# Optimization experiments

Measured on AMD Instinct MI355X. Metric: run time of the kernel, lower is better.

## Reference

```python
import jax, jax.numpy as jnp
import numpy as np

B, S, D = 4, 2048, 768
H = 12
HD = D // H  # 64


def setup_inputs() -> dict:
    key = jax.random.key(0)
    ks = jax.random.split(key, 7)
    scale = 1.0 / np.sqrt(D)
    return {
        "hidden_states": jax.random.normal(ks[0], (B, S, D), dtype=jnp.float32),
        "Wq": jax.random.normal(ks[1], (D, D), dtype=jnp.float32) * scale,
        "bq": jnp.zeros((D,), dtype=jnp.float32),
        "Wk": jax.random.normal(ks[2], (D, D), dtype=jnp.float32) * scale,
        "bk": jnp.zeros((D,), dtype=jnp.float32),
        "Wv": jax.random.normal(ks[3], (D, D), dtype=jnp.float32) * scale,
        "bv": jnp.zeros((D,), dtype=jnp.float32),
    }


def _split_heads(x):
    # [B, S, D] -> [B, H, S, HD]
    b, s, _ = x.shape
    return x.reshape(b, s, H, HD).transpose(0, 2, 1, 3)


def reference(hidden_states, Wq, bq, Wk, bk, Wv, bv):
    q = _split_heads(hidden_states @ Wq + bq)
    k = _split_heads(hidden_states @ Wk + bk)
    v = _split_heads(hidden_states @ Wv + bv)
    # [B, H, S, S] attention scores (naive full materialization, as in source)
    scores = jnp.einsum("bhqd,bhkd->bhqk", q, k) / jnp.sqrt(jnp.float32(HD))
    attn = jax.nn.softmax(scores, axis=-1)  # dropout = identity (eval)
    ctx = jnp.einsum("bhqk,bhkd->bhqd", attn, v)
    # [B, H, S, HD] -> [B, S, D]
    return ctx.transpose(0, 2, 1, 3).reshape(hidden_states.shape[0], -1, H * HD)
```

## Files before the change

### kernel.cpp

```cpp
#include <hip/hip_runtime.h>
#include <cmath>

#define B_  4
#define S_  2048
#define D_  768
#define H_  12
#define HD_ 64
#define BH_ 48
#define N3_ 2304
#define M_  8192

typedef _Float16 half8  __attribute__((ext_vector_type(8)));
typedef _Float16 half4v __attribute__((ext_vector_type(4)));
typedef __fp16   fp16x2 __attribute__((ext_vector_type(2)));
typedef __fp16   fp16x4 __attribute__((ext_vector_type(4)));
typedef float    floatx4 __attribute__((ext_vector_type(4)));

typedef const unsigned int __attribute__((address_space(1)))* gas_u32;
typedef unsigned int __attribute__((address_space(3)))* las_u32;

#define LOG2E 1.4426950408889634f
#define NEG_C (-5.0f * 1.4426950408889634f)

__global__ void cvt_f32_f16(const float* __restrict__ src,
                            _Float16* __restrict__ dst, int n) {
  int i = (blockIdx.x * blockDim.x + threadIdx.x) * 4;
  if (i < n) {
    float4 v = *(const float4*)(src + i);
    half4v h = {(_Float16)v.x, (_Float16)v.y, (_Float16)v.z, (_Float16)v.w};
    *(half4v*)(dst + i) = h;
  }
}

__global__ __launch_bounds__(256) void transpose_cvt_w(
    const float* __restrict__ W, _Float16* __restrict__ Wt) {
  __shared__ float tile[32][33];
  const int k0 = blockIdx.x * 32, n0 = blockIdx.y * 32;
  const int r = threadIdx.x >> 3, c4 = (threadIdx.x & 7) * 4;
  float4 v = *(const float4*)(W + (size_t)(k0 + r) * D_ + n0 + c4);
  tile[r][c4 + 0] = v.x; tile[r][c4 + 1] = v.y;
  tile[r][c4 + 2] = v.z; tile[r][c4 + 3] = v.w;
  __syncthreads();
  half4v h = {(_Float16)tile[c4 + 0][r], (_Float16)tile[c4 + 1][r],
              (_Float16)tile[c4 + 2][r], (_Float16)tile[c4 + 3][r]};
  *(half4v*)(Wt + (size_t)(n0 + r) * D_ + k0 + c4) = h;
}

__global__ __launch_bounds__(256, 3) void gemm_qkv(
    const _Float16* __restrict__ Xh, const _Float16* __restrict__ Wt3,
    const float* __restrict__ bq, const float* __restrict__ bk,
    const float* __restrict__ bv,
    _Float16* __restrict__ qo, _Float16* __restrict__ ko,
    _Float16* __restrict__ vto) {
  __shared__ __align__(16) char gsm[36864];
  _Float16* As = (_Float16*)gsm;
  _Float16* Bs = (_Float16*)(gsm + 16384);
  const int tid = threadIdx.x;
  const int w = tid >> 6, lane = tid & 63;
  const int tx = lane & 15, quad = lane >> 4;
  const int nBase = blockIdx.x * 128;
  const int mBase = blockIdx.y * 128;
  const int wm = (w & 1) * 64, wn = (w >> 1) * 64;

  floatx4 acc[4][4];
  #pragma unroll
  for (int i = 0; i < 4; ++i)
    #pragma unroll
    for (int j = 0; j < 4; ++j) acc[i][j] = (floatx4){0.f, 0.f, 0.f, 0.f};

  const int ldRow = lane >> 3;
  const int ldCol = (lane & 7) * 8;

  for (int k0 = 0; k0 < D_; k0 += 64) {
    __syncthreads();
    #pragma unroll
    for (int io = 0; io < 4; ++io) {
      int row = w * 32 + io * 8;
      const _Float16* ga =
          Xh + (size_t)(mBase + row + ldRow) * D_ + k0 + ldCol;
      __builtin_amdgcn_global_load_lds((gas_u32)(const void*)ga,
                                       (las_u32)(void*)&As[row * 64], 16, 0, 0);
      const _Float16* gb =
          Wt3 + (size_t)(nBase + row + ldRow) * D_ + k0 + ldCol;
      __builtin_amdgcn_global_load_lds((gas_u32)(const void*)gb,
                                       (las_u32)(void*)&Bs[row * 64], 16, 0, 0);
    }
    __syncthreads();

    half8 af0[4], af1[4], bf0[4], bf1[4];
    #pragma unroll
    for (int i = 0; i < 4; ++i) {
      af0[i] = *(const half8*)&As[(wm + 16 * i + tx) * 64 + quad * 8];
      af1[i] = *(const half8*)&As[(wm + 16 * i + tx) * 64 + quad * 8 + 32];
    }
    #pragma unroll
    for (int j = 0; j < 4; ++j) {
      bf0[j] = *(const half8*)&Bs[(wn + 16 * j + tx) * 64 + quad * 8];
      bf1[j] = *(const half8*)&Bs[(wn + 16 * j + tx) * 64 + quad * 8 + 32];
    }
    #pragma unroll
    for (int i = 0; i < 4; ++i)
      #pragma unroll
      for (int j = 0; j < 4; ++j) {
        acc[i][j] = __builtin_amdgcn_mfma_f32_16x16x32_f16(af0[i], bf0[j], acc[i][j], 0, 0, 0);
        acc[i][j] = __builtin_amdgcn_mfma_f32_16x16x32_f16(af1[i], bf1[j], acc[i][j], 0, 0, 0);
      }
  }

  const int region = nBase / 768;
  const int b = mBase >> 11;
  const int sBase = mBase & (S_ - 1);

  if (region < 2) {
    const float scale = (region == 0) ? 0.125f * LOG2E : 1.0f;
    const float* bias = (region == 0) ? bq : bk;
    _Float16* dst = (region == 0) ? qo : ko;
    const int nLoc768 = nBase % 768;
    __syncthreads();
    _Float16 (*Ct)[136] = (_Float16(*)[136])gsm;
    #pragma unroll
    for (int j = 0; j < 4; ++j) {
      int nl = wn + 16 * j + tx;
      float bb = bias[nLoc768 + nl];
      #pragma unroll
      for (int i = 0; i < 4; ++i)
        #pragma unroll
        for (int r = 0; r < 4; ++r)
          Ct[wm + 16 * i + quad * 4 + r][nl] = (_Float16)((acc[i][j][r] + bb) * scale);
    }
    __syncthreads();
    #pragma unroll
    for (int io = 0; io < 8; ++io) {
      int idx = io * 256 + tid;
      int ml = idx >> 4;
      int nc = (idx & 15) * 8;
      int n = nLoc768 + nc, h = n >> 6, d = n & 63;
      half8 hv = *(const half8*)&Ct[ml][nc];
      *(half8*)(dst + ((size_t)(b * H_ + h) * S_ + sBase + ml) * HD_ + d) = hv;
    }
  } else {
    __syncthreads();
    _Float16 (*Ct)[144] = (_Float16(*)[144])gsm;
    const int nV = nBase - 1536;
    #pragma unroll
    for (int j = 0; j < 4; ++j) {
      int nl = wn + 16 * j + tx;
      float bb = bv[nV + nl];
      #pragma unroll
      for (int i = 0; i < 4; ++i)
        #pragma unroll
        for (int r = 0; r < 4; ++r)
          Ct[nl][wm + 16 * i + quad * 4 + r] = (_Float16)(acc[i][j][r] + bb);
    }
    __syncthreads();
    #pragma unroll
    for (int io = 0; io < 8; ++io) {
      int idx = io * 256 + tid;
      int nl = idx >> 4;
      int sc = (idx & 15) * 8;
      int n = nV + nl, h = n >> 6, d = n & 63;
      half8 hv = *(const half8*)&Ct[nl][sc];
      *(half8*)(vto + (((size_t)(b * H_ + h) * HD_) + d) * S_ + sBase + sc) = hv;
    }
  }
}

__global__ __launch_bounds__(512, 4) void attn_mfma(
    const _Float16* __restrict__ qh, const _Float16* __restrict__ kh,
    const _Float16* __restrict__ vth, float* __restrict__ out) {
  __shared__ __align__(16) char smem[36864];
  _Float16 (*Ks2)[64][72]  = (_Float16(*)[64][72])smem;
  _Float16 (*Vts2)[64][72] = (_Float16(*)[64][72])(smem + 18432);
  float (*Of)[68] = (float(*)[68])smem;
  float* lbuf = (float*)(smem + 34816);

  const int tid = threadIdx.x;
  const int bh = blockIdx.y;
  const int qBase = blockIdx.x * 128;
  const int w = tid >> 6, lane = tid & 63;
  const int half = w >> 2, wq = w & 3;
  const int tx = lane & 15, quad = lane >> 4;

  const _Float16* kp = kh + (size_t)bh * S_ * HD_;
  const _Float16* vtp = vth + (size_t)bh * HD_ * S_;

  half8 bq[2][2];
  #pragma unroll
  for (int g = 0; g < 2; ++g) {
    const _Float16* qp =
        qh + ((size_t)bh * S_ + qBase + wq * 32 + g * 16 + tx) * HD_;
    bq[g][0] = *(const half8*)(qp + quad * 8);
    bq[g][1] = *(const half8*)(qp + quad * 8 + 32);
  }

  floatx4 o_acc[2][4];
  #pragma unroll
  for (int g = 0; g < 2; ++g)
    #pragma unroll
    for (int j = 0; j < 4; ++j) o_acc[g][j] = (floatx4){0.f, 0.f, 0.f, 0.f};
  float l_loc[2] = {0.f, 0.f};

  const int th = tid & 255;
  const int kr = th >> 3, kc = (th & 7) * 8;

  for (int it = 0; it < S_ / 128; ++it) {
    const int kt0 = it * 128 + half * 64;
    __syncthreads();
    #pragma unroll
    for (int io = 0; io < 2; ++io) {
      int row = kr + io * 32;
      *(half8*)&Ks2[half][row][kc] =
          *(const half8*)(kp + (size_t)(kt0 + row) * HD_ + kc);
      *(half8*)&Vts2[half][row][kc] =
          *(const half8*)(vtp + (size_t)row * S_ + kt0 + kc);
    }
    __syncthreads();

    #pragma unroll
    for (int t = 0; t < 4; ++t) {
      half8 ka0 = *(const half8*)&Ks2[half][16 * t + tx][quad * 8];
      half8 ka1 = *(const half8*)&Ks2[half][16 * t + tx][quad * 8 + 32];
      fp16x4 pf[2];
      #pragma unroll
      for (int g = 0; g < 2; ++g) {
        __builtin_amdgcn_s_setprio(1);
        floatx4 st = __builtin_amdgcn_mfma_f32_16x16x32_f16(
            ka0, bq[g][0], (floatx4){NEG_C, NEG_C, NEG_C, NEG_C}, 0, 0, 0);
        st = __builtin_amdgcn_mfma_f32_16x16x32_f16(ka1, bq[g][1], st, 0, 0, 0);
        __builtin_amdgcn_s_setprio(0);
        float p0 = __builtin_amdgcn_exp2f(st[0]);
        float p1 = __builtin_amdgcn_exp2f(st[1]);
        float p2 = __builtin_amdgcn_exp2f(st[2]);
        float p3 = __builtin_amdgcn_exp2f(st[3]);
        l_loc[g] += (p0 + p1) + (p2 + p3);
        fp16x2 lo = __builtin_amdgcn_cvt_pkrtz(p0, p1);
        fp16x2 hi = __builtin_amdgcn_cvt_pkrtz(p2, p3);
        pf[g] = (fp16x4){lo.x, lo.y, hi.x, hi.y};
      }
      __builtin_amdgcn_s_setprio(1);
      #pragma unroll
      for (int j = 0; j < 4; ++j) {
        fp16x4 vb = *(const fp16x4*)&Vts2[half][16 * j + tx][16 * t + quad * 4];
        o_acc[0][j] = __builtin_amdgcn_mfma_f32_16x16x16f16(pf[0], vb, o_acc[0][j], 0, 0, 0);
        o_acc[1][j] = __builtin_amdgcn_mfma_f32_16x16x16f16(pf[1], vb, o_acc[1][j], 0, 0, 0);
      }
      __builtin_amdgcn_s_setprio(0);
    }
  }

  float lg[2];
  #pragma unroll
  for (int g = 0; g < 2; ++g) {
    lg[g] = l_loc[g];
    lg[g] += __shfl_xor(lg[g], 16, 64);
    lg[g] += __shfl_xor(lg[g], 32, 64);
  }

  __syncthreads();
  if (half == 1) {
    #pragma unroll
    for (int g = 0; g < 2; ++g) {
      int rowB = wq * 32 + g * 16;
      #pragma unroll
      for (int j = 0; j < 4; ++j)
        #pragma unroll
        for (int r = 0; r < 4; ++r)
          Of[rowB + quad * 4 + r][16 * j + tx] = o_acc[g][j][r];
      if (quad == 0) lbuf[rowB + tx] = lg[g];
    }
  }
  __syncthreads();
  if (half == 0) {
    const int b = bh / H_;
    const int h = bh % H_;
    #pragma unroll
    for (int g = 0; g < 2; ++g) {
      int rowB = wq * 32 + g * 16;
      float ltot = lg[g] + lbuf[rowB + tx];
      #pragma unroll
      for (int r = 0; r < 4; ++r) {
        int m = quad * 4 + r;
        float inv = 1.f / __shfl(ltot, m, 64);
        int s = qBase + rowB + m;
        #pragma unroll
        for (int j = 0; j < 4; ++j) {
          float o = o_acc[g][j][r] + Of[rowB + m][16 * j + tx];
          out[((size_t)b * S_ + s) * D_ + h * HD_ + 16 * j + tx] = o * inv;
        }
      }
    }
  }
}

extern "C" void kernel_launch(void* const* d_in, const int* in_sizes, int n_in,
                              void* d_out, int out_size, void* d_ws, size_t ws_size,
                              hipStream_t stream) {
  const float* X  = (const float*)d_in[0];
  const float* Wq = (const float*)d_in[1];
  const float* bq = (const float*)d_in[2];
  const float* Wk = (const float*)d_in[3];
  const float* bk = (const float*)d_in[4];
  const float* Wv = (const float*)d_in[5];
  const float* bv = (const float*)d_in[6];
  float* out = (float*)d_out;

  const size_t nX = (size_t)M_ * D_;
  const size_t nW = (size_t)D_ * D_;
  const size_t nQ = (size_t)BH_ * S_ * HD_;

  _Float16* Xh  = (_Float16*)d_ws;
  _Float16* Wt3 = Xh + nX;
  _Float16* qhb = Wt3 + 3 * nW;
  _Float16* khb = qhb + nQ;
  _Float16* vtb = khb + nQ;

  cvt_f32_f16<<<(int)(nX / 4 / 256), 256, 0, stream>>>(X, Xh, (int)nX);

  dim3 gridT(D_ / 32, D_ / 32);
  transpose_cvt_w<<<gridT, 256, 0, stream>>>(Wq, Wt3);
  transpose_cvt_w<<<gridT, 256, 0, stream>>>(Wk, Wt3 + nW);
  transpose_cvt_w<<<gridT, 256, 0, stream>>>(Wv, Wt3 + 2 * nW);

  dim3 gridG(N3_ / 128, M_ / 128);
  gemm_qkv<<<gridG, 256, 0, stream>>>(Xh, Wt3, bq, bk, bv, qhb, khb, vtb);

  dim3 gridA(S_ / 128, BH_);
  attn_mfma<<<gridA, 512, 0, stream>>>(qhb, khb, vtb, out);
}
```

Before: 212.7 us.

## Register-prefetch next K/V tile in attention loop and merge weight transposes

The attention kernel now loads the next K and V^T tile from global memory into registers while the current tile is being computed, then writes them to shared memory at the start of the next iteration. This hides global load latency behind the MFMA and softmax work. The three weight transpose-convert launches are merged into a single launch with a z-dimension selecting the matrix, which saves two kernel launches. The cost is extra registers per thread, which could reduce occupancy.

```diff
diff --git a/kernel.cpp b/kernel.cpp
--- a/kernel.cpp
+++ b/kernel.cpp
@@ -32,9 +32,13 @@
   }
 }
 
-__global__ __launch_bounds__(256) void transpose_cvt_w(
-    const float* __restrict__ W, _Float16* __restrict__ Wt) {
+__global__ __launch_bounds__(256) void transpose_cvt_w3(
+    const float* __restrict__ Wq, const float* __restrict__ Wk,
+    const float* __restrict__ Wv, _Float16* __restrict__ Wt3) {
   __shared__ float tile[32][33];
+  const int which = blockIdx.z;
+  const float* W = (which == 0) ? Wq : (which == 1) ? Wk : Wv;
+  _Float16* Wt = Wt3 + (size_t)which * D_ * D_;
   const int k0 = blockIdx.x * 32, n0 = blockIdx.y * 32;
   const int r = threadIdx.x >> 3, c4 = (threadIdx.x & 7) * 4;
   float4 v = *(const float4*)(W + (size_t)(k0 + r) * D_ + n0 + c4);
@@ -203,16 +207,34 @@
   const int th = tid & 255;
   const int kr = th >> 3, kc = (th & 7) * 8;
 
-  for (int it = 0; it < S_ / 128; ++it) {
-    const int kt0 = it * 128 + half * 64;
-    __syncthreads();
+  const int NT = S_ / 128;
+  half8 kst[2], vst[2];
+  {
+    const int kt0 = half * 64;
     #pragma unroll
     for (int io = 0; io < 2; ++io) {
       int row = kr + io * 32;
-      *(half8*)&Ks2[half][row][kc] =
-          *(const half8*)(kp + (size_t)(kt0 + row) * HD_ + kc);
-      *(half8*)&Vts2[half][row][kc] =
-          *(const half8*)(vtp + (size_t)row * S_ + kt0 + kc);
+      kst[io] = *(const half8*)(kp + (size_t)(kt0 + row) * HD_ + kc);
+      vst[io] = *(const half8*)(vtp + (size_t)row * S_ + kt0 + kc);
+    }
+  }
+
+  for (int it = 0; it < NT; ++it) {
+    __syncthreads();
+    #pragma unroll
+    for (int io = 0; io < 2; ++io) {
+      int row = kr + io * 32;
+      *(half8*)&Ks2[half][row][kc] = kst[io];
+      *(half8*)&Vts2[half][row][kc] = vst[io];
+    }
+    if (it + 1 < NT) {
+      const int kt1 = (it + 1) * 128 + half * 64;
+      #pragma unroll
+      for (int io = 0; io < 2; ++io) {
+        int row = kr + io * 32;
+        kst[io] = *(const half8*)(kp + (size_t)(kt1 + row) * HD_ + kc);
+        vst[io] = *(const half8*)(vtp + (size_t)row * S_ + kt1 + kc);
+      }
     }
     __syncthreads();
 
@@ -316,10 +338,8 @@
 
   cvt_f32_f16<<<(int)(nX / 4 / 256), 256, 0, stream>>>(X, Xh, (int)nX);
 
-  dim3 gridT(D_ / 32, D_ / 32);
-  transpose_cvt_w<<<gridT, 256, 0, stream>>>(Wq, Wt3);
-  transpose_cvt_w<<<gridT, 256, 0, stream>>>(Wk, Wt3 + nW);
-  transpose_cvt_w<<<gridT, 256, 0, stream>>>(Wv, Wt3 + 2 * nW);
+  dim3 gridT(D_ / 32, D_ / 32, 3);
+  transpose_cvt_w3<<<gridT, 256, 0, stream>>>(Wq, Wk, Wv, Wt3);
 
   dim3 gridG(N3_ / 128, M_ / 128);
   gemm_qkv<<<gridG, 256, 0, stream>>>(Xh, Wt3, bq, bk, bv, qhb, khb, vtb);
```

Measured after the change: 205.8 us. 3.2% less time.
